# Kernel tuning notes

Measured on AMD Instinct MI355X. Metric: run time of the kernel, lower is better.

## Reference

```python
import jax, jax.numpy as jnp
import numpy as np

D_MODEL = 1024


def setup_inputs() -> dict:
    key = jax.random.key(0)
    ks = jax.random.split(key, 8)
    B, S, D = 2, 2048, D_MODEL
    s = 1.0 / np.sqrt(D)
    causal = jnp.where(jnp.tril(jnp.ones((S, S), dtype=bool)), 0.0, -1e9)[None, None]
    return {
        "query": jax.random.normal(ks[0], (B, S, D), jnp.float32),
        "key": jax.random.normal(ks[1], (B, S, D), jnp.float32),
        "value": jax.random.normal(ks[2], (B, S, D), jnp.float32),
        "padding_mask": jnp.zeros((B, 1, 1, S), jnp.float32),
        "lookahead_mask": causal.astype(jnp.float32),
        "w_q": jax.random.normal(ks[3], (D, D), jnp.float32) * s,
        "w_k": jax.random.normal(ks[4], (D, D), jnp.float32) * s,
        "w_v": jax.random.normal(ks[5], (D, D), jnp.float32) * s,
        "w_out": jax.random.normal(ks[6], (D, D), jnp.float32) * s,
        "b_q": jnp.zeros((D,), jnp.float32),
        "b_k": jnp.zeros((D,), jnp.float32),
        "b_v": jnp.zeros((D,), jnp.float32),
        "b_out": jnp.zeros((D,), jnp.float32),
        "n_heads": 16,
    }


def reference(query, key, value, padding_mask, lookahead_mask,
              w_q, w_k, w_v, w_out, b_q, b_k, b_v, b_out, n_heads):
    B, S, D = query.shape
    d_k = D // n_heads
    # projections (torch Linear: x @ W.T + b; here weights stored as (in, out))
    q = (query @ w_q + b_q).reshape(B, S, n_heads, d_k).transpose(0, 2, 1, 3)
    k = (key @ w_k + b_k).reshape(B, S, n_heads, d_k).transpose(0, 2, 1, 3)
    v = (value @ w_v + b_v).reshape(B, S, n_heads, d_k).transpose(0, 2, 1, 3)
    scores = jnp.einsum("bhqd,bhkd->bhqk", q, k) / jnp.sqrt(jnp.float32(d_k))
    scores = scores + padding_mask + lookahead_mask
    attn = jax.nn.softmax(scores, axis=-1)
    out = jnp.einsum("bhqk,bhkd->bhqd", attn, v)
    out = out.transpose(0, 2, 1, 3).reshape(B, S, D)
    return out @ w_out + b_out
```

## Files before the change

kernel.cpp:

```cpp
#include <hip/hip_runtime.h>
#include <hip/hip_bf16.h>
#include <stdint.h>

typedef __bf16 bf16x8 __attribute__((ext_vector_type(8)));
typedef __bf16 bf16x4 __attribute__((ext_vector_type(4)));
typedef float f32x4 __attribute__((ext_vector_type(4)));

#define DMODEL 1024
#define SEQ    2048
#define NHEAD  16
#define DK     64
#define MTOT   4096
#define KDIM   1024

#define DRAIN_VM_LGKM() asm volatile("s_waitcnt vmcnt(0) lgkmcnt(0)" ::: "memory")
#define DRAIN_LGKM()    asm volatile("s_waitcnt lgkmcnt(0)" ::: "memory")

__device__ __forceinline__ void gl2lds16(const void* g, void* l) {
  __builtin_amdgcn_global_load_lds((__attribute__((address_space(1))) void*)(g),
                                   (__attribute__((address_space(3))) void*)(l),
                                   16, 0, 0);
}

__global__ __launch_bounds__(256) void k_cvt3(const float* __restrict__ q,
                                              const float* __restrict__ k,
                                              const float* __restrict__ v,
                                              __bf16* __restrict__ oq,
                                              __bf16* __restrict__ ok,
                                              __bf16* __restrict__ ov,
                                              int n4) {
  const int which = blockIdx.y;
  const float* in = which == 0 ? q : (which == 1 ? k : v);
  __bf16* out = which == 0 ? oq : (which == 1 ? ok : ov);
  const int i = blockIdx.x * 256 + threadIdx.x;
  if (i >= n4) return;
  const float4 f = ((const float4*)in)[i];
  bf16x4 o = { (__bf16)f.x, (__bf16)f.y, (__bf16)f.z, (__bf16)f.w };
  ((bf16x4*)out)[i] = o;
}

__global__ __launch_bounds__(256) void k_transpose4(const float* __restrict__ w0,
                                                    const float* __restrict__ w1,
                                                    const float* __restrict__ w2,
                                                    const float* __restrict__ w3,
                                                    __bf16* __restrict__ t0,
                                                    __bf16* __restrict__ t1,
                                                    __bf16* __restrict__ t2,
                                                    __bf16* __restrict__ t3) {
  const int z = blockIdx.z;
  const float* W = z == 0 ? w0 : (z == 1 ? w1 : (z == 2 ? w2 : w3));
  __bf16* WT = z == 0 ? t0 : (z == 1 ? t1 : (z == 2 ? t2 : t3));
  __shared__ float tile[32][33];
  int n0 = blockIdx.x * 32, k0 = blockIdx.y * 32;
  int tx = threadIdx.x & 31, ty = threadIdx.x >> 5;
  #pragma unroll
  for (int i = ty; i < 32; i += 8)
    tile[i][tx] = W[(size_t)(k0 + i) * DMODEL + n0 + tx];
  __syncthreads();
  #pragma unroll
  for (int i = ty; i < 32; i += 8)
    WT[(size_t)(n0 + i) * DMODEL + k0 + tx] = (__bf16)tile[tx][i];
}

__global__ __launch_bounds__(256) void k_gemm_qkv(
    const __bf16* __restrict__ A0, const __bf16* __restrict__ A1, const __bf16* __restrict__ A2,
    const __bf16* __restrict__ W0, const __bf16* __restrict__ W1, const __bf16* __restrict__ W2,
    const float* __restrict__ bi0, const float* __restrict__ bi1, const float* __restrict__ bi2,
    __bf16* __restrict__ C0, __bf16* __restrict__ C1, __bf16* __restrict__ C2) {
  const int z = blockIdx.z;
  const __bf16* A  = z == 0 ? A0 : (z == 1 ? A1 : A2);
  const __bf16* BT = z == 0 ? W0 : (z == 1 ? W1 : W2);
  const float* bias = z == 0 ? bi0 : (z == 1 ? bi1 : bi2);
  __bf16* Cout = z == 0 ? C0 : (z == 1 ? C1 : C2);

  __shared__ __align__(16) __bf16 As[128 * 32];
  __shared__ __align__(16) __bf16 Bs[128 * 32];
  const int tid = threadIdx.x;
  const int lane = tid & 63;
  const int wv = tid >> 6;
  const int wm = wv >> 1, wn = wv & 1;
  const int m0 = blockIdx.y * 128, n0 = blockIdx.x * 128;
  const int lr = lane & 15, lg = lane >> 4;

  f32x4 acc[4][4] = {};

  for (int k0 = 0; k0 < KDIM; k0 += 32) {
    #pragma unroll
    for (int i = 0; i < 2; ++i) {
      int c = tid + i * 256;
      int row = c >> 2, seg = c & 3;
      gl2lds16(A + (size_t)(m0 + row) * KDIM + k0 + seg * 8, (char*)As + c * 16);
      gl2lds16(BT + (size_t)(n0 + row) * KDIM + k0 + seg * 8, (char*)Bs + c * 16);
    }
    DRAIN_VM_LGKM();
    __syncthreads();
    bf16x8 af[4], bfr[4];
    #pragma unroll
    for (int mi = 0; mi < 4; ++mi)
      af[mi] = *(const bf16x8*)&As[(wm * 64 + mi * 16 + lr) * 32 + lg * 8];
    #pragma unroll
    for (int ni = 0; ni < 4; ++ni)
      bfr[ni] = *(const bf16x8*)&Bs[(wn * 64 + ni * 16 + lr) * 32 + lg * 8];
    #pragma unroll
    for (int mi = 0; mi < 4; ++mi)
      #pragma unroll
      for (int ni = 0; ni < 4; ++ni)
        acc[mi][ni] = __builtin_amdgcn_mfma_f32_16x16x32_bf16(af[mi], bfr[ni], acc[mi][ni], 0, 0, 0);
    DRAIN_LGKM();
    __syncthreads();
  }

  #pragma unroll
  for (int mi = 0; mi < 4; ++mi)
    #pragma unroll
    for (int ni = 0; ni < 4; ++ni) {
      const int col = n0 + wn * 64 + ni * 16 + lr;
      const float bv = bias[col];
      #pragma unroll
      for (int r = 0; r < 4; ++r) {
        const int row = m0 + wm * 64 + mi * 16 + lg * 4 + r;
        float v = acc[mi][ni][r] + bv;
        const int b = row >> 11, s = row & (SEQ - 1);
        const int h = col >> 6, dd = col & (DK - 1);
        if (z == 2)
          Cout[((size_t)(b * NHEAD + h) * DK + dd) * SEQ + s] = (__bf16)v;
        else
          Cout[((size_t)(b * NHEAD + h) * SEQ + s) * DK + dd] = (__bf16)v;
      }
    }
}

__global__ __launch_bounds__(256) void k_gemm_out(const __bf16* __restrict__ A,
                                                  const __bf16* __restrict__ BT,
                                                  const float* __restrict__ bias,
                                                  float* __restrict__ Cout) {
  __shared__ __align__(16) __bf16 As[128 * 32];
  __shared__ __align__(16) __bf16 Bs[128 * 32];
  const int tid = threadIdx.x;
  const int lane = tid & 63;
  const int wv = tid >> 6;
  const int wm = wv >> 1, wn = wv & 1;
  const int m0 = blockIdx.y * 128, n0 = blockIdx.x * 128;
  const int lr = lane & 15, lg = lane >> 4;

  f32x4 acc[4][4] = {};

  for (int k0 = 0; k0 < KDIM; k0 += 32) {
    #pragma unroll
    for (int i = 0; i < 2; ++i) {
      int c = tid + i * 256;
      int row = c >> 2, seg = c & 3;
      gl2lds16(A + (size_t)(m0 + row) * KDIM + k0 + seg * 8, (char*)As + c * 16);
      gl2lds16(BT + (size_t)(n0 + row) * KDIM + k0 + seg * 8, (char*)Bs + c * 16);
    }
    DRAIN_VM_LGKM();
    __syncthreads();
    bf16x8 af[4], bfr[4];
    #pragma unroll
    for (int mi = 0; mi < 4; ++mi)
      af[mi] = *(const bf16x8*)&As[(wm * 64 + mi * 16 + lr) * 32 + lg * 8];
    #pragma unroll
    for (int ni = 0; ni < 4; ++ni)
      bfr[ni] = *(const bf16x8*)&Bs[(wn * 64 + ni * 16 + lr) * 32 + lg * 8];
    #pragma unroll
    for (int mi = 0; mi < 4; ++mi)
      #pragma unroll
      for (int ni = 0; ni < 4; ++ni)
        acc[mi][ni] = __builtin_amdgcn_mfma_f32_16x16x32_bf16(af[mi], bfr[ni], acc[mi][ni], 0, 0, 0);
    DRAIN_LGKM();
    __syncthreads();
  }

  #pragma unroll
  for (int mi = 0; mi < 4; ++mi)
    #pragma unroll
    for (int ni = 0; ni < 4; ++ni) {
      const int col = n0 + wn * 64 + ni * 16 + lr;
      const float bv = bias[col];
      #pragma unroll
      for (int r = 0; r < 4; ++r) {
        const int row = m0 + wm * 64 + mi * 16 + lg * 4 + r;
        Cout[(size_t)row * DMODEL + col] = acc[mi][ni][r] + bv;
      }
    }
}

__global__ __launch_bounds__(256, 4) void k_attn(const __bf16* __restrict__ Q,
                                                 const __bf16* __restrict__ Kt,
                                                 const __bf16* __restrict__ Vt,
                                                 const float* __restrict__ pmask,
                                                 float* __restrict__ Op0,
                                                 float* __restrict__ Op1,
                                                 float* __restrict__ ML) {
  __shared__ __align__(16) __bf16 Ks[2][64 * 64];
  __shared__ __align__(16) __bf16 Vs[2][64 * 64];
  __shared__ __align__(16) __bf16 plds[4][16 * 64];

  const int tid = threadIdx.x;
  const int lane = tid & 63, wv = tid >> 6;
  const int lr = lane & 15, lg = lane >> 4;

  const int bid = blockIdx.x;
  const int xcd = bid & 7;
  const int rdec = bid >> 3;
  const int slot = rdec >> 5;
  const int rem = rdec & 31;
  const int pair = rem >> 1;
  const int s = rem & 1;
  const int bh = slot * 8 + xcd;
  const int b = bh >> 4, h = bh & 15;

  const __bf16* Qb = Q + (size_t)bh * SEQ * DK;
  const __bf16* Kb = Kt + (size_t)bh * SEQ * DK;
  const __bf16* Vb = Vt + (size_t)bh * DK * SEQ;
  const float* pm = pmask + (size_t)b * SEQ;
  float* Op = s ? Op1 : Op0;
  const float SCL = 0.125f * 1.44269504f;
  const float L2E = 1.44269504f;

  auto stage = [&](int buf, int t) {
    #pragma unroll
    for (int i = 0; i < 2; ++i) {
      const int c = tid + i * 256;
      const int row = c >> 3;
      const int sx = ((c & 7) * 16) ^ ((row & 7) << 4);
      gl2lds16((const char*)Kb + (size_t)(t * 64 + row) * 128 + sx,
               (char*)&Ks[buf][0] + c * 16);
      gl2lds16((const char*)Vb + (size_t)row * (SEQ * 2) + (size_t)t * 128 + sx,
               (char*)&Vs[buf][0] + c * 16);
    }
  };

  for (int half = 0; half < 2; ++half) {
    const int qb = half ? (31 - pair) : pair;
    const int nt = qb + 1;
    const int QR = qb * 64 + wv * 16;

    const bf16x8 qf0 = *(const bf16x8*)&Qb[(size_t)(QR + lr) * DK + lg * 8];
    const bf16x8 qf1 = *(const bf16x8*)&Qb[(size_t)(QR + lr) * DK + 32 + lg * 8];

    float mrow = -1e30f, lrw = 0.f;
    f32x4 oacc[4] = {};

    int t = s;
    if (t < nt) {
      stage(0, t);
      DRAIN_VM_LGKM();
      __syncthreads();
    }
    int cur = 0;
    for (; t < nt; t += 2) {
      if (t + 2 < nt) stage(cur ^ 1, t + 2);
      f32x4 sc[4];
      #pragma unroll
      for (int g = 0; g < 4; ++g) {
        const int krow = g * 16 + lr;
        const int ksw = (lr & 7) << 4;
        bf16x8 kf0 = *(const bf16x8*)((const char*)&Ks[cur][0] + krow * 128 + ((lg * 16) ^ ksw));
        bf16x8 kf1 = *(const bf16x8*)((const char*)&Ks[cur][0] + krow * 128 + ((64 + lg * 16) ^ ksw));
        f32x4 a = {};
        a = __builtin_amdgcn_mfma_f32_16x16x32_bf16(kf0, qf0, a, 0, 0, 0);
        a = __builtin_amdgcn_mfma_f32_16x16x32_bf16(kf1, qf1, a, 0, 0, 0);
        sc[g] = a;
      }
      const bool edge = (t == qb);
      #pragma unroll
      for (int g = 0; g < 4; ++g) {
        const float4 pmv = *(const float4*)&pm[t * 64 + g * 16 + lg * 4];
        const float pmf[4] = {pmv.x, pmv.y, pmv.z, pmv.w};
        #pragma unroll
        for (int r = 0; r < 4; ++r) {
          float sv = sc[g][r] * SCL + pmf[r] * L2E;
          if (edge && (t * 64 + g * 16 + lg * 4 + r > QR + lr)) sv = -1e30f;
          sc[g][r] = sv;
        }
      }
      float pmax = sc[0][0];
      #pragma unroll
      for (int g = 0; g < 4; ++g)
        #pragma unroll
        for (int r = 0; r < 4; ++r) pmax = fmaxf(pmax, sc[g][r]);
      pmax = fmaxf(pmax, __shfl_xor(pmax, 16, 64));
      pmax = fmaxf(pmax, __shfl_xor(pmax, 32, 64));
      if (!__all(pmax <= mrow + 8.f)) {
        const float mnew = fmaxf(mrow, pmax);
        const float alpha = exp2f(mrow - mnew);
        mrow = mnew;
        lrw *= alpha;
        #pragma unroll
        for (int r = 0; r < 4; ++r) {
          const float av = __shfl(alpha, lg * 4 + r, 64);
          #pragma unroll
          for (int og = 0; og < 4; ++og) oacc[og][r] *= av;
        }
      }
      float psum = 0.f;
      #pragma unroll
      for (int g = 0; g < 4; ++g)
        #pragma unroll
        for (int r = 0; r < 4; ++r) {
          float p = exp2f(sc[g][r] - mrow);
          sc[g][r] = p;
          psum += p;
        }
      psum += __shfl_xor(psum, 16, 64);
      psum += __shfl_xor(psum, 32, 64);
      lrw += psum;
      #pragma unroll
      for (int g = 0; g < 4; ++g) {
        bf16x4 pk = { (__bf16)sc[g][0], (__bf16)sc[g][1], (__bf16)sc[g][2], (__bf16)sc[g][3] };
        const int byteoff = lr * 128 + ((g * 32 + lg * 8) ^ ((lr & 7) << 4));
        *(bf16x4*)((char*)plds[wv] + byteoff) = pk;
      }
      #pragma unroll
      for (int kk = 0; kk < 2; ++kk) {
        const int pboff = lr * 128 + ((kk * 64 + lg * 16) ^ ((lr & 7) << 4));
        const bf16x8 pa = *(const bf16x8*)((char*)plds[wv] + pboff);
        #pragma unroll
        for (int og = 0; og < 4; ++og) {
          const int vrow = og * 16 + lr;
          const int vsw = (vrow & 7) << 4;
          const bf16x8 vf = *(const bf16x8*)((const char*)&Vs[cur][0] + vrow * 128 + ((kk * 64 + lg * 16) ^ vsw));
          oacc[og] = __builtin_amdgcn_mfma_f32_16x16x32_bf16(pa, vf, oacc[og], 0, 0, 0);
        }
      }
      DRAIN_VM_LGKM();
      __syncthreads();
      cur ^= 1;
    }

    #pragma unroll
    for (int r = 0; r < 4; ++r) {
      const int row = QR + lg * 4 + r;
      #pragma unroll
      for (int og = 0; og < 4; ++og)
        Op[((size_t)b * SEQ + row) * DMODEL + h * DK + og * 16 + lr] = oacc[og][r];
    }
    if (lg == 0) {
      const int ri = bh * SEQ + QR + lr;
      ML[s * 131072 + ri] = mrow;
      ML[s * 131072 + 65536 + ri] = lrw;
    }
  }
}

__global__ __launch_bounds__(256) void k_merge(const float* __restrict__ Op0,
                                               const float* __restrict__ Op1,
                                               const float* __restrict__ ML,
                                               __bf16* __restrict__ Oh) {
  const int idx = blockIdx.x * 256 + threadIdx.x;
  const int row = idx >> 8;
  const int col = (idx & 255) * 4;
  const int b = row >> 11, sr = row & (SEQ - 1);
  const int h = col >> 6;
  const int ri = (b * NHEAD + h) * SEQ + sr;
  const float m0 = ML[ri], l0 = ML[65536 + ri];
  const float m1 = ML[131072 + ri], l1 = ML[196608 + ri];
  const float M = fmaxf(m0, m1);
  const float w0 = exp2f(m0 - M), w1 = exp2f(m1 - M);
  const float inv = 1.f / (l0 * w0 + l1 * w1);
  const float s0 = w0 * inv, s1 = w1 * inv;
  const size_t off = (size_t)row * DMODEL + col;
  const float4 o0 = *(const float4*)&Op0[off];
  const float4 o1 = *(const float4*)&Op1[off];
  bf16x4 o = { (__bf16)(o0.x * s0 + o1.x * s1), (__bf16)(o0.y * s0 + o1.y * s1),
               (__bf16)(o0.z * s0 + o1.z * s1), (__bf16)(o0.w * s0 + o1.w * s1) };
  *(bf16x4*)&Oh[off] = o;
}

extern "C" void kernel_launch(void* const* d_in, const int* in_sizes, int n_in,
                              void* d_out, int out_size, void* d_ws, size_t ws_size,
                              hipStream_t stream) {
  (void)in_sizes; (void)n_in; (void)out_size; (void)ws_size;
  const float* query = (const float*)d_in[0];
  const float* key   = (const float*)d_in[1];
  const float* value = (const float*)d_in[2];
  const float* pmask = (const float*)d_in[3];
  const float* w_q = (const float*)d_in[5];
  const float* w_k = (const float*)d_in[6];
  const float* w_v = (const float*)d_in[7];
  const float* w_o = (const float*)d_in[8];
  const float* b_q = (const float*)d_in[9];
  const float* b_k = (const float*)d_in[10];
  const float* b_v = (const float*)d_in[11];
  const float* b_o = (const float*)d_in[12];

  __bf16* ws = (__bf16*)d_ws;
  const size_t WSZ = (size_t)DMODEL * DMODEL;
  const size_t XSZ = (size_t)MTOT * DMODEL;
  __bf16* WTq = ws;
  __bf16* WTk = WTq + WSZ;
  __bf16* WTv = WTk + WSZ;
  __bf16* WTo = WTv + WSZ;
  __bf16* Xq  = WTo + WSZ;
  __bf16* Xk  = Xq + XSZ;
  __bf16* Xv  = Xk + XSZ;
  __bf16* Qh  = Xv + XSZ;
  __bf16* Kh  = Qh + XSZ;
  __bf16* Vh  = Kh + XSZ;
  float*  Op0 = (float*)Xk;
  float*  Op1 = (float*)(Vh + XSZ);
  float*  MLb = (float*)(Vh + XSZ + 2 * XSZ);
  __bf16* Oh  = Xq;

  dim3 blk(256);
  k_cvt3<<<dim3(4096, 3), blk, 0, stream>>>(query, key, value, Xq, Xk, Xv, (int)(XSZ / 4));
  k_transpose4<<<dim3(32, 32, 4), blk, 0, stream>>>(w_q, w_k, w_v, w_o, WTq, WTk, WTv, WTo);

  k_gemm_qkv<<<dim3(8, 32, 3), blk, 0, stream>>>(Xq, Xk, Xv, WTq, WTk, WTv,
                                                 b_q, b_k, b_v, Qh, Kh, Vh);

  k_attn<<<dim3(1024), blk, 0, stream>>>(Qh, Kh, Vh, pmask, Op0, Op1, MLb);
  k_merge<<<dim3(4096), blk, 0, stream>>>(Op0, Op1, MLb, Oh);

  k_gemm_out<<<dim3(8, 32), blk, 0, stream>>>(Oh, WTo, b_o, (float*)d_out);
}
```

Measured before the change: 151.9 us.

## Merge prep kernels, deepen GEMM K-tile with swizzled LDS, store partials in bf16

Folds the input conversion and weight transpose into one launch, doubles the GEMM K-step to 64 and adds an XOR-swizzled LDS layout. Attention partial outputs are now stored as bf16 instead of fp32, which halves their write and read traffic in the merge. This cuts launch overhead, halves barriers per GEMM, and avoids LDS bank conflicts, at the cost of more LDS per block and extra rounding of the unnormalised partial sums.

```diff
diff --git a/kernel.cpp b/kernel.cpp
--- a/kernel.cpp
+++ b/kernel.cpp
@@ -22,44 +22,46 @@
                                    16, 0, 0);
 }
 
-__global__ __launch_bounds__(256) void k_cvt3(const float* __restrict__ q,
+__global__ __launch_bounds__(256) void k_prep(const float* __restrict__ q,
                                               const float* __restrict__ k,
                                               const float* __restrict__ v,
                                               __bf16* __restrict__ oq,
                                               __bf16* __restrict__ ok,
                                               __bf16* __restrict__ ov,
-                                              int n4) {
-  const int which = blockIdx.y;
-  const float* in = which == 0 ? q : (which == 1 ? k : v);
-  __bf16* out = which == 0 ? oq : (which == 1 ? ok : ov);
-  const int i = blockIdx.x * 256 + threadIdx.x;
-  if (i >= n4) return;
-  const float4 f = ((const float4*)in)[i];
-  bf16x4 o = { (__bf16)f.x, (__bf16)f.y, (__bf16)f.z, (__bf16)f.w };
-  ((bf16x4*)out)[i] = o;
-}
-
-__global__ __launch_bounds__(256) void k_transpose4(const float* __restrict__ w0,
-                                                    const float* __restrict__ w1,
-                                                    const float* __restrict__ w2,
-                                                    const float* __restrict__ w3,
-                                                    __bf16* __restrict__ t0,
-                                                    __bf16* __restrict__ t1,
-                                                    __bf16* __restrict__ t2,
-                                                    __bf16* __restrict__ t3) {
-  const int z = blockIdx.z;
-  const float* W = z == 0 ? w0 : (z == 1 ? w1 : (z == 2 ? w2 : w3));
-  __bf16* WT = z == 0 ? t0 : (z == 1 ? t1 : (z == 2 ? t2 : t3));
+                                              const float* __restrict__ w0,
+                                              const float* __restrict__ w1,
+                                              const float* __restrict__ w2,
+                                              const float* __restrict__ w3,
+                                              __bf16* __restrict__ t0,
+                                              __bf16* __restrict__ t1,
+                                              __bf16* __restrict__ t2,
+                                              __bf16* __restrict__ t3) {
   __shared__ float tile[32][33];
-  int n0 = blockIdx.x * 32, k0 = blockIdx.y * 32;
-  int tx = threadIdx.x & 31, ty = threadIdx.x >> 5;
-  #pragma unroll
-  for (int i = ty; i < 32; i += 8)
-    tile[i][tx] = W[(size_t)(k0 + i) * DMODEL + n0 + tx];
-  __syncthreads();
-  #pragma unroll
-  for (int i = ty; i < 32; i += 8)
-    WT[(size_t)(n0 + i) * DMODEL + k0 + tx] = (__bf16)tile[tx][i];
+  const int bid = blockIdx.x;
+  if (bid < 12288) {
+    const int which = bid >> 12;
+    const int i = (bid & 4095) * 256 + threadIdx.x;
+    const float* in = which == 0 ? q : (which == 1 ? k : v);
+    __bf16* out = which == 0 ? oq : (which == 1 ? ok : ov);
+    const float4 f = ((const float4*)in)[i];
+    bf16x4 o = { (__bf16)f.x, (__bf16)f.y, (__bf16)f.z, (__bf16)f.w };
+    ((bf16x4*)out)[i] = o;
+  } else {
+    const int b2 = bid - 12288;
+    const int z = b2 >> 10;
+    const int t = b2 & 1023;
+    const float* W = z == 0 ? w0 : (z == 1 ? w1 : (z == 2 ? w2 : w3));
+    __bf16* WT = z == 0 ? t0 : (z == 1 ? t1 : (z == 2 ? t2 : t3));
+    const int n0 = (t & 31) * 32, k0 = (t >> 5) * 32;
+    const int tx = threadIdx.x & 31, ty = threadIdx.x >> 5;
+    #pragma unroll
+    for (int i = ty; i < 32; i += 8)
+      tile[i][tx] = W[(size_t)(k0 + i) * DMODEL + n0 + tx];
+    __syncthreads();
+    #pragma unroll
+    for (int i = ty; i < 32; i += 8)
+      WT[(size_t)(n0 + i) * DMODEL + k0 + tx] = (__bf16)tile[tx][i];
+  }
 }
 
 __global__ __launch_bounds__(256) void k_gemm_qkv(
@@ -73,8 +75,8 @@
   const float* bias = z == 0 ? bi0 : (z == 1 ? bi1 : bi2);
   __bf16* Cout = z == 0 ? C0 : (z == 1 ? C1 : C2);
 
-  __shared__ __align__(16) __bf16 As[128 * 32];
-  __shared__ __align__(16) __bf16 Bs[128 * 32];
+  __shared__ __align__(16) __bf16 As[128 * 64];
+  __shared__ __align__(16) __bf16 Bs[128 * 64];
   const int tid = threadIdx.x;
   const int lane = tid & 63;
   const int wv = tid >> 6;
@@ -84,28 +86,33 @@
 
   f32x4 acc[4][4] = {};
 
-  for (int k0 = 0; k0 < KDIM; k0 += 32) {
-    #pragma unroll
-    for (int i = 0; i < 2; ++i) {
-      int c = tid + i * 256;
-      int row = c >> 2, seg = c & 3;
-      gl2lds16(A + (size_t)(m0 + row) * KDIM + k0 + seg * 8, (char*)As + c * 16);
-      gl2lds16(BT + (size_t)(n0 + row) * KDIM + k0 + seg * 8, (char*)Bs + c * 16);
+  for (int k0 = 0; k0 < KDIM; k0 += 64) {
+    #pragma unroll
+    for (int i = 0; i < 4; ++i) {
+      const int c = tid + i * 256;
+      const int row = c >> 3, seg = c & 7;
+      const int sx = (seg * 16) ^ ((row & 7) << 4);
+      gl2lds16((const char*)A + ((size_t)(m0 + row) * KDIM + k0) * 2 + sx, (char*)As + c * 16);
+      gl2lds16((const char*)BT + ((size_t)(n0 + row) * KDIM + k0) * 2 + sx, (char*)Bs + c * 16);
     }
     DRAIN_VM_LGKM();
     __syncthreads();
-    bf16x8 af[4], bfr[4];
-    #pragma unroll
-    for (int mi = 0; mi < 4; ++mi)
-      af[mi] = *(const bf16x8*)&As[(wm * 64 + mi * 16 + lr) * 32 + lg * 8];
-    #pragma unroll
-    for (int ni = 0; ni < 4; ++ni)
-      bfr[ni] = *(const bf16x8*)&Bs[(wn * 64 + ni * 16 + lr) * 32 + lg * 8];
-    #pragma unroll
-    for (int mi = 0; mi < 4; ++mi)
+    const int ksw = (lr & 7) << 4;
+    #pragma unroll
+    for (int hh = 0; hh < 2; ++hh) {
+      bf16x8 af[4], bfr[4];
+      #pragma unroll
+      for (int mi = 0; mi < 4; ++mi)
+        af[mi] = *(const bf16x8*)((const char*)As + (wm * 64 + mi * 16 + lr) * 128 + ((hh * 64 + lg * 16) ^ ksw));
       #pragma unroll
       for (int ni = 0; ni < 4; ++ni)
-        acc[mi][ni] = __builtin_amdgcn_mfma_f32_16x16x32_bf16(af[mi], bfr[ni], acc[mi][ni], 0, 0, 0);
+        bfr[ni] = *(const bf16x8*)((const char*)Bs + (wn * 64 + ni * 16 + lr) * 128 + ((hh * 64 + lg * 16) ^ ksw));
+      #pragma unroll
+      for (int mi = 0; mi < 4; ++mi)
+        #pragma unroll
+        for (int ni = 0; ni < 4; ++ni)
+          acc[mi][ni] = __builtin_amdgcn_mfma_f32_16x16x32_bf16(af[mi], bfr[ni], acc[mi][ni], 0, 0, 0);
+    }
     DRAIN_LGKM();
     __syncthreads();
   }
@@ -134,8 +141,8 @@
                                                   const __bf16* __restrict__ BT,
                                                   const float* __restrict__ bias,
                                                   float* __restrict__ Cout) {
-  __shared__ __align__(16) __bf16 As[128 * 32];
-  __shared__ __align__(16) __bf16 Bs[128 * 32];
+  __shared__ __align__(16) __bf16 As[128 * 64];
+  __shared__ __align__(16) __bf16 Bs[128 * 64];
   const int tid = threadIdx.x;
   const int lane = tid & 63;
   const int wv = tid >> 6;
@@ -145,28 +152,33 @@
 
   f32x4 acc[4][4] = {};
 
-  for (int k0 = 0; k0 < KDIM; k0 += 32) {
-    #pragma unroll
-    for (int i = 0; i < 2; ++i) {
-      int c = tid + i * 256;
-      int row = c >> 2, seg = c & 3;
-      gl2lds16(A + (size_t)(m0 + row) * KDIM + k0 + seg * 8, (char*)As + c * 16);
-      gl2lds16(BT + (size_t)(n0 + row) * KDIM + k0 + seg * 8, (char*)Bs + c * 16);
+  for (int k0 = 0; k0 < KDIM; k0 += 64) {
+    #pragma unroll
+    for (int i = 0; i < 4; ++i) {
+      const int c = tid + i * 256;
+      const int row = c >> 3, seg = c & 7;
+      const int sx = (seg * 16) ^ ((row & 7) << 4);
+      gl2lds16((const char*)A + ((size_t)(m0 + row) * KDIM + k0) * 2 + sx, (char*)As + c * 16);
+      gl2lds16((const char*)BT + ((size_t)(n0 + row) * KDIM + k0) * 2 + sx, (char*)Bs + c * 16);
     }
     DRAIN_VM_LGKM();
     __syncthreads();
-    bf16x8 af[4], bfr[4];
-    #pragma unroll
-    for (int mi = 0; mi < 4; ++mi)
-      af[mi] = *(const bf16x8*)&As[(wm * 64 + mi * 16 + lr) * 32 + lg * 8];
-    #pragma unroll
-    for (int ni = 0; ni < 4; ++ni)
-      bfr[ni] = *(const bf16x8*)&Bs[(wn * 64 + ni * 16 + lr) * 32 + lg * 8];
-    #pragma unroll
-    for (int mi = 0; mi < 4; ++mi)
+    const int ksw = (lr & 7) << 4;
+    #pragma unroll
+    for (int hh = 0; hh < 2; ++hh) {
+      bf16x8 af[4], bfr[4];
+      #pragma unroll
+      for (int mi = 0; mi < 4; ++mi)
+        af[mi] = *(const bf16x8*)((const char*)As + (wm * 64 + mi * 16 + lr) * 128 + ((hh * 64 + lg * 16) ^ ksw));
       #pragma unroll
       for (int ni = 0; ni < 4; ++ni)
-        acc[mi][ni] = __builtin_amdgcn_mfma_f32_16x16x32_bf16(af[mi], bfr[ni], acc[mi][ni], 0, 0, 0);
+        bfr[ni] = *(const bf16x8*)((const char*)Bs + (wn * 64 + ni * 16 + lr) * 128 + ((hh * 64 + lg * 16) ^ ksw));
+      #pragma unroll
+      for (int mi = 0; mi < 4; ++mi)
+        #pragma unroll
+        for (int ni = 0; ni < 4; ++ni)
+          acc[mi][ni] = __builtin_amdgcn_mfma_f32_16x16x32_bf16(af[mi], bfr[ni], acc[mi][ni], 0, 0, 0);
+    }
     DRAIN_LGKM();
     __syncthreads();
   }
@@ -189,8 +201,8 @@
                                                  const __bf16* __restrict__ Kt,
                                                  const __bf16* __restrict__ Vt,
                                                  const float* __restrict__ pmask,
-                                                 float* __restrict__ Op0,
-                                                 float* __restrict__ Op1,
+                                                 __bf16* __restrict__ Op0,
+                                                 __bf16* __restrict__ Op1,
                                                  float* __restrict__ ML) {
   __shared__ __align__(16) __bf16 Ks[2][64 * 64];
   __shared__ __align__(16) __bf16 Vs[2][64 * 64];
@@ -214,7 +226,7 @@
   const __bf16* Kb = Kt + (size_t)bh * SEQ * DK;
   const __bf16* Vb = Vt + (size_t)bh * DK * SEQ;
   const float* pm = pmask + (size_t)b * SEQ;
-  float* Op = s ? Op1 : Op0;
+  __bf16* Op = s ? Op1 : Op0;
   const float SCL = 0.125f * 1.44269504f;
   const float L2E = 1.44269504f;
 
@@ -334,7 +346,7 @@
       const int row = QR + lg * 4 + r;
       #pragma unroll
       for (int og = 0; og < 4; ++og)
-        Op[((size_t)b * SEQ + row) * DMODEL + h * DK + og * 16 + lr] = oacc[og][r];
+        Op[((size_t)b * SEQ + row) * DMODEL + h * DK + og * 16 + lr] = (__bf16)oacc[og][r];
     }
     if (lg == 0) {
       const int ri = bh * SEQ + QR + lr;
@@ -344,8 +356,8 @@
   }
 }
 
-__global__ __launch_bounds__(256) void k_merge(const float* __restrict__ Op0,
-                                               const float* __restrict__ Op1,
+__global__ __launch_bounds__(256) void k_merge(const __bf16* __restrict__ Op0,
+                                               const __bf16* __restrict__ Op1,
                                                const float* __restrict__ ML,
                                                __bf16* __restrict__ Oh) {
   const int idx = blockIdx.x * 256 + threadIdx.x;
@@ -361,10 +373,12 @@
   const float inv = 1.f / (l0 * w0 + l1 * w1);
   const float s0 = w0 * inv, s1 = w1 * inv;
   const size_t off = (size_t)row * DMODEL + col;
-  const float4 o0 = *(const float4*)&Op0[off];
-  const float4 o1 = *(const float4*)&Op1[off];
-  bf16x4 o = { (__bf16)(o0.x * s0 + o1.x * s1), (__bf16)(o0.y * s0 + o1.y * s1),
-               (__bf16)(o0.z * s0 + o1.z * s1), (__bf16)(o0.w * s0 + o1.w * s1) };
+  const bf16x4 o0 = *(const bf16x4*)&Op0[off];
+  const bf16x4 o1 = *(const bf16x4*)&Op1[off];
+  bf16x4 o = { (__bf16)((float)o0[0] * s0 + (float)o1[0] * s1),
+               (__bf16)((float)o0[1] * s0 + (float)o1[1] * s1),
+               (__bf16)((float)o0[2] * s0 + (float)o1[2] * s1),
+               (__bf16)((float)o0[3] * s0 + (float)o1[3] * s1) };
   *(bf16x4*)&Oh[off] = o;
 }
 
@@ -398,14 +412,14 @@
   __bf16* Qh  = Xv + XSZ;
   __bf16* Kh  = Qh + XSZ;
   __bf16* Vh  = Kh + XSZ;
-  float*  Op0 = (float*)Xk;
-  float*  Op1 = (float*)(Vh + XSZ);
-  float*  MLb = (float*)(Vh + XSZ + 2 * XSZ);
+  __bf16* Op0 = Xk;
+  __bf16* Op1 = Xv;
+  float*  MLb = (float*)(Vh + XSZ);
   __bf16* Oh  = Xq;
 
   dim3 blk(256);
-  k_cvt3<<<dim3(4096, 3), blk, 0, stream>>>(query, key, value, Xq, Xk, Xv, (int)(XSZ / 4));
-  k_transpose4<<<dim3(32, 32, 4), blk, 0, stream>>>(w_q, w_k, w_v, w_o, WTq, WTk, WTv, WTo);
+  k_prep<<<dim3(16384), blk, 0, stream>>>(query, key, value, Xq, Xk, Xv,
+                                          w_q, w_k, w_v, w_o, WTq, WTk, WTv, WTo);
 
   k_gemm_qkv<<<dim3(8, 32, 3), blk, 0, stream>>>(Xq, Xk, Xv, WTq, WTk, WTv,
                                                  b_q, b_k, b_v, Qh, Kh, Vh);
```

Result: slower. 161.2 us (+6.2%).
